# Performance work log

Measured on AMD Instinct MI355X. Metric: run time of the kernel, lower is better.

Reference implementation:

```python
import jax, jax.numpy as jnp
import numpy as np
from jax import lax

B, C_IN, L = 512, 32, 512
E = 8
POOL = 16            # AdaptiveAvgPool1d(16)
D_IN = C_IN * L      # expert input = flattened x
D_OUT = 768          # pooler_output dim (hard-coded in module)
TAU = 1.0            # gumbel temperature
BN_EPS = 1e-5


def setup_inputs() -> dict:
    key = jax.random.key(0)
    ks = jax.random.split(key, 8)
    s = 0.02
    return {
        "x": jax.random.normal(ks[0], (B, C_IN, L), jnp.float32),
        "gumbel_u": jax.random.uniform(ks[1], (B, E), jnp.float32, 1e-6, 1.0 - 1e-6),
        "conv_w": jax.random.normal(ks[2], (64, C_IN, 3), jnp.float32) * s,
        "conv_b": jnp.zeros((64,), jnp.float32),
        "bn_gamma": jnp.ones((64 * POOL,), jnp.float32),
        "bn_beta": jnp.zeros((64 * POOL,), jnp.float32),
        "bn_mean": jnp.zeros((64 * POOL,), jnp.float32),
        "bn_var": jnp.ones((64 * POOL,), jnp.float32),
        "fc1_w": jax.random.normal(ks[3], (128, 64 * POOL), jnp.float32) * s,
        "fc1_b": jnp.zeros((128,), jnp.float32),
        "fc2_w": jax.random.normal(ks[4], (E, 128), jnp.float32) * s,
        "fc2_b": jnp.zeros((E,), jnp.float32),
        "expert_w": jax.random.normal(ks[5], (E, D_IN, D_OUT), jnp.float32) * s,
        "expert_b": jnp.zeros((E, D_OUT), jnp.float32),
    }


def _gelu(v):
    return jax.nn.gelu(v, approximate=False)  # torch nn.GELU default (erf)


def reference(x, gumbel_u, conv_w, conv_b, bn_gamma, bn_beta, bn_mean, bn_var,
              fc1_w, fc1_b, fc2_w, fc2_b, expert_w, expert_b):
    # ---- router ----
    h = lax.conv_general_dilated(x, conv_w, (1,), ((1, 1),),
                                 dimension_numbers=("NCH", "OIH", "NCH"))
    h = _gelu(h + conv_b[None, :, None])                     # [B,64,L]
    h = h.reshape(B, 64, POOL, L // POOL).mean(-1)           # adaptive avg pool -> [B,64,16]
    h = h.reshape(B, 64 * POOL)                              # flatten
    h = (h - bn_mean) * lax.rsqrt(bn_var + BN_EPS) * bn_gamma + bn_beta  # BN (eval)
    h = _gelu(h @ fc1_w.T + fc1_b)                           # dropout inactive in eval
    logits = h @ fc2_w.T + fc2_b                             # [B,E]

    # ---- soft gumbel-softmax gating (hard=False), then top-2 ----
    g = -jnp.log(-jnp.log(gumbel_u))
    routing_weights = jax.nn.softmax((logits + g) / TAU, axis=1)
    topv, topi = lax.top_k(routing_weights, 2)               # [B,2]
    w = topv / (topv.sum(axis=1, keepdims=True) + 1e-8)      # [B,2]

    # ---- dispatch/compute/combine (dense-expert stand-in: flatten + linear) ----
    xf = x.reshape(B, D_IN)
    all_out = jnp.einsum("bd,edh->beh", xf, expert_w) + expert_b[None]  # [B,E,768]
    sel = jnp.take_along_axis(all_out, topi[:, :, None], axis=1)        # [B,2,768]
    pooler_output = (sel * w[:, :, None]).sum(axis=1)                   # [B,768]
    return pooler_output
```

## Files before the change

kernel.cpp:

```cpp
#include <hip/hip_runtime.h>
#include <hip/hip_bf16.h>

#define NB 512
#define CIN 32
#define LEN 512
#define NE 8
#define NPOOL 16
#define DIN 16384
#define DOUT 768
#define HD 1024
#define F1 128

#define MT 256
#define NT 64
#define BK 32
#define NBUF 4

typedef __attribute__((ext_vector_type(4))) float f32x4;
typedef __attribute__((ext_vector_type(8))) short s16x8;
typedef __attribute__((ext_vector_type(4))) unsigned int u32x4;

__device__ __forceinline__ float gelu_erf(float v) {
    return 0.5f * v * (1.0f + erff(v * 0.70710678118654752f));
}

__device__ __forceinline__ unsigned cvt_pk(float lo, float hi) {
    unsigned r;
    asm volatile("v_cvt_pk_bf16_f32 %0, %1, %2" : "=v"(r) : "v"(lo), "v"(hi));
    return r;
}

__device__ __forceinline__ unsigned short f2bf_u(float f) {
    union { float f; unsigned u; } x; x.f = f;
    unsigned r = x.u + 0x7fffu + ((x.u >> 16) & 1u);
    return (unsigned short)(r >> 16);
}

__device__ __forceinline__ void gload_lds16(const void* gptr, void* lptr) {
    __builtin_amdgcn_global_load_lds(
        (const __attribute__((address_space(1))) unsigned int*)gptr,
        (__attribute__((address_space(3))) unsigned int*)lptr,
        16, 0, 0);
}

__global__ __launch_bounds__(256) void krouter_conv(
    const float* __restrict__ x, const float* __restrict__ cw, const float* __restrict__ cb,
    const float* __restrict__ bng, const float* __restrict__ bnb,
    const float* __restrict__ bnm, const float* __restrict__ bnv,
    float* __restrict__ h, int* __restrict__ cnt)
{
    __shared__ float xs[CIN * 264];
    int half = blockIdx.x;
    int b = blockIdx.y;
    int t = threadIdx.x;
    if (b == 0 && half == 0 && t < NE) cnt[t] = 0;

    int Lchunk0 = half * 64 - 1;
    const float* xb_ = x + (size_t)b * DIN;
    for (int idx = t; idx < CIN * 66; idx += 256) {
        int ci = idx / 66;
        int cc = idx - ci * 66;
        int gc = min(max(Lchunk0 + cc, 0), 127);
        f32x4 v = *(const f32x4*)(xb_ + ci * 512 + gc * 4);
        int byte = ci * 1056 + ((cc << 4) ^ (((cc >> 3) & 7) << 4));
        *(f32x4*)((char*)xs + byte) = v;
    }
    __syncthreads();

    int p  = t & 7;
    int pg = half * 8 + p;
    int cq = t >> 3;
    int co0 = cq * 2, co1 = co0 + 1;

    float sa[32], sb[32];
    #pragma unroll
    for (int i = 0; i < 32; ++i) { sa[i] = 0.f; sb[i] = 0.f; }

    for (int ci = 0; ci < CIN; ++ci) {
        float f[40];
        #pragma unroll
        for (int u = 0; u < 10; ++u) {
            int lc = p * 8 + u;
            int byte = ci * 1056 + ((lc << 4) ^ (((lc >> 3) & 7) << 4));
            f32x4 v = *(const f32x4*)((const char*)xs + byte);
            f[4*u+0] = v[0]; f[4*u+1] = v[1]; f[4*u+2] = v[2]; f[4*u+3] = v[3];
        }
        if (pg == 0)  f[3]  = 0.f;
        if (pg == 15) f[36] = 0.f;
        float wa0 = cw[co0*96 + ci*3 + 0], wa1 = cw[co0*96 + ci*3 + 1], wa2 = cw[co0*96 + ci*3 + 2];
        float wb0 = cw[co1*96 + ci*3 + 0], wb1 = cw[co1*96 + ci*3 + 1], wb2 = cw[co1*96 + ci*3 + 2];
        #pragma unroll
        for (int i = 0; i < 32; ++i) {
            sa[i] = fmaf(f[i+3], wa0, fmaf(f[i+4], wa1, fmaf(f[i+5], wa2, sa[i])));
            sb[i] = fmaf(f[i+3], wb0, fmaf(f[i+4], wb1, fmaf(f[i+5], wb2, sb[i])));
        }
    }

    float ba = cb[co0], bbv = cb[co1];
    float ma = 0.f, mb = 0.f;
    #pragma unroll
    for (int i = 0; i < 32; ++i) { ma += gelu_erf(sa[i] + ba); mb += gelu_erf(sb[i] + bbv); }
    ma *= (1.f / 32.f); mb *= (1.f / 32.f);

    int oa = co0 * NPOOL + pg, ob = co1 * NPOOL + pg;
    float ra = (ma - bnm[oa]) * rsqrtf(bnv[oa] + 1e-5f) * bng[oa] + bnb[oa];
    float rb = (mb - bnm[ob]) * rsqrtf(bnv[ob] + 1e-5f) * bng[ob] + bnb[ob];
    h[(size_t)b * HD + oa] = ra;
    h[(size_t)b * HD + ob] = rb;
}

__global__ __launch_bounds__(256) void krouter_fc(
    const float* __restrict__ h, const float* __restrict__ f1w, const float* __restrict__ f1b,
    const float* __restrict__ f2w, const float* __restrict__ f2b,
    const float* __restrict__ gu,
    int* __restrict__ top2e, float* __restrict__ top2w,
    int* __restrict__ cnt, int* __restrict__ rowlist, float* __restrict__ roww)
{
    __shared__ float hs[8 * HD];
    __shared__ float h1s[8 * F1];
    __shared__ float lg[8 * NE];

    int bb = blockIdx.x * 8;
    int t = threadIdx.x;

    const f32x4* hg = (const f32x4*)(h + (size_t)bb * HD);
    f32x4* hs4 = (f32x4*)hs;
    #pragma unroll
    for (int u = 0; u < 8; ++u) hs4[t + 256 * u] = hg[t + 256 * u];
    __syncthreads();

    int j = t & 127;
    int pr = t >> 7;
    float acc[4] = {0.f, 0.f, 0.f, 0.f};
    const f32x4* w4 = (const f32x4*)(f1w + (size_t)j * HD);
    for (int k4 = 0; k4 < 256; ++k4) {
        f32x4 w = w4[k4];
        #pragma unroll
        for (int g = 0; g < 4; ++g) {
            f32x4 hv = hs4[(pr * 4 + g) * 256 + k4];
            acc[g] += w[0]*hv[0] + w[1]*hv[1] + w[2]*hv[2] + w[3]*hv[3];
        }
    }
    float bj = f1b[j];
    #pragma unroll
    for (int g = 0; g < 4; ++g) h1s[(pr * 4 + g) * F1 + j] = gelu_erf(acc[g] + bj);
    __syncthreads();

    if (t < 64) {
        int bi = t >> 3, e = t & 7;
        float s = f2b[e];
        const float* w = f2w + e * F1;
        const float* hh = h1s + bi * F1;
        #pragma unroll 8
        for (int k = 0; k < F1; ++k) s += hh[k] * w[k];
        lg[bi * NE + e] = s;
    }
    __syncthreads();

    if (t < 8) {
        int bi = t; int b = bb + bi;
        float r[NE];
        float mx = -1e30f;
        #pragma unroll
        for (int e = 0; e < NE; ++e) {
            float g = -logf(-logf(gu[b * NE + e]));
            r[e] = lg[bi * NE + e] + g;
            mx = fmaxf(mx, r[e]);
        }
        float sum = 0.f;
        #pragma unroll
        for (int e = 0; e < NE; ++e) { r[e] = expf(r[e] - mx); sum += r[e]; }
        float inv = 1.f / sum;
        #pragma unroll
        for (int e = 0; e < NE; ++e) r[e] *= inv;
        int e0 = 0; float v0 = r[0];
        #pragma unroll
        for (int e = 1; e < NE; ++e) if (r[e] > v0) { v0 = r[e]; e0 = e; }
        int e1 = -1; float v1 = -1.f;
        #pragma unroll
        for (int e = 0; e < NE; ++e) { if (e == e0) continue; if (r[e] > v1) { v1 = r[e]; e1 = e; } }
        float den = v0 + v1 + 1e-8f;
        float w0 = v0 / den, w1 = v1 / den;
        top2e[b * 2 + 0] = e0; top2e[b * 2 + 1] = e1;
        top2w[b * 2 + 0] = w0; top2w[b * 2 + 1] = w1;
        int p0 = atomicAdd(&cnt[e0], 1);
        rowlist[e0 * NB + p0] = b * 2 + 0; roww[e0 * NB + p0] = w0;
        int p1 = atomicAdd(&cnt[e1], 1);
        rowlist[e1 * NB + p1] = b * 2 + 1; roww[e1 * NB + p1] = w1;
    }
}

__global__ __launch_bounds__(512, 4) void kgemm(
    const float* __restrict__ x, const float* __restrict__ ew,
    const int* __restrict__ cnt, const int* __restrict__ rowlist, const float* __restrict__ roww,
    unsigned short* __restrict__ ypart, int nkc, int kch)
{
    int nwg = gridDim.x;
    int cpx = nwg >> 3;
    int wg = (blockIdx.x & 7) * cpx + (blockIdx.x >> 3);
    int nt = wg % 12;
    int kc = (wg / 12) % nkc;
    int e  = wg / (12 * nkc);
    int cn = cnt[e];
    if (cn <= 0) return;

    __shared__ __align__(16) char As[2][MT * 64];
    __shared__ __align__(16) char Bs[NBUF][BK * NT * 4];

    int t = threadIdx.x;
    int wid = t >> 6, lane = t & 63;
    int wm = wid >> 1, wn = wid & 1;
    int g = lane >> 4;
    int NS = kch / BK;
    int k0 = kc * kch;

    const char* gB = (const char*)ew + (size_t)e * DIN * DOUT * 4
                   + (size_t)k0 * (DOUT * 4) + nt * NT * 4;
    int bk_ = wid * 4 + (lane >> 4);
    int bc_ = lane & 15;
    int bkey = ((bk_ >> 3) & 3) << 2;
    const char* gp = gB + (size_t)bk_ * (DOUT * 4) + ((bc_ ^ bkey) << 4);
    int ldsB = wid * 1024;

    int arow = t >> 1, ah = t & 1;
    int akey = (arow ^ (arow >> 2)) & 3;
    int aw0 = arow * 64 + (((2 * ah) ^ akey) << 4);
    int aw1 = arow * 64 + (((2 * ah + 1) ^ akey) << 4);

    for (int row0 = 0; row0 < cn; row0 += MT) {
        int mloc = min(MT, cn - row0);
        bool wact = (wm * 64 < mloc);

        int arc = min(arow, mloc - 1);
        const float* axp = x + (size_t)(rowlist[e * NB + row0 + arc] >> 1) * DIN
                         + k0 + ah * 16;

        f32x4 acc[4][2];
        #pragma unroll
        for (int i = 0; i < 4; ++i)
            #pragma unroll
            for (int jj = 0; jj < 2; ++jj) acc[i][jj] = (f32x4){0.f, 0.f, 0.f, 0.f};

        f32x4 An[4];
        const char* bp = gp;

        auto loadA = [&](int s) {
            const f32x4* p = (const f32x4*)(axp + (size_t)s * BK);
            An[0] = p[0]; An[1] = p[1]; An[2] = p[2]; An[3] = p[3];
        };
        auto stageB = [&](int s) {
            gload_lds16(bp + (size_t)s * ((size_t)BK * DOUT * 4),
                        (char*)Bs[s & (NBUF - 1)] + ldsB);
        };
        auto writeA = [&](int bi) {
            u32x4 q0, q1;
            q0[0] = cvt_pk(An[0][0], An[0][1]); q0[1] = cvt_pk(An[0][2], An[0][3]);
            q0[2] = cvt_pk(An[1][0], An[1][1]); q0[3] = cvt_pk(An[1][2], An[1][3]);
            q1[0] = cvt_pk(An[2][0], An[2][1]); q1[1] = cvt_pk(An[2][2], An[2][3]);
            q1[2] = cvt_pk(An[3][0], An[3][1]); q1[3] = cvt_pk(An[3][2], An[3][3]);
            *(u32x4*)(As[bi] + aw0) = q0;
            *(u32x4*)(As[bi] + aw1) = q1;
        };

        loadA(0);
        stageB(0);
        if (NS > 1) stageB(1);
        writeA(0);

        for (int s = 0; s < NS; ++s) {
            if (s + 1 < NS) loadA(s + 1);
            if (s + 2 < NS) stageB(s + 2);
            __builtin_amdgcn_sched_barrier(0);
            if (s + 2 < NS)      asm volatile("s_waitcnt vmcnt(6) lgkmcnt(0)" ::: "memory");
            else if (s + 1 < NS) asm volatile("s_waitcnt vmcnt(5) lgkmcnt(0)" ::: "memory");
            else                 asm volatile("s_waitcnt vmcnt(0) lgkmcnt(0)" ::: "memory");
            __builtin_amdgcn_sched_barrier(0);
            __builtin_amdgcn_s_barrier();
            __builtin_amdgcn_sched_barrier(0);

            if (wact) {
                const char* Ab = As[s & 1];
                const char* Bb = Bs[s & (NBUF - 1)];
                __builtin_amdgcn_s_setprio(1);
                s16x8 af[4];
                #pragma unroll
                for (int mi = 0; mi < 4; ++mi) {
                    int m = wm * 64 + mi * 16 + (lane & 15);
                    int key = (m ^ (m >> 2)) & 3;
                    af[mi] = *(const s16x8*)(Ab + m * 64 + ((g ^ key) << 4));
                }
                #pragma unroll
                for (int ni = 0; ni < 2; ++ni) {
                    int n = wn * 32 + ni * 16 + (lane & 15);
                    int cb = (((n >> 2) ^ (g << 2)) << 4) + ((n & 3) << 2);
                    float v[8];
                    #pragma unroll
                    for (int j = 0; j < 8; ++j)
                        v[j] = *(const float*)(Bb + (g * 8 + j) * 256 + cb);
                    union { u32x4 u; s16x8 v8; } bf;
                    bf.u[0] = cvt_pk(v[0], v[1]); bf.u[1] = cvt_pk(v[2], v[3]);
                    bf.u[2] = cvt_pk(v[4], v[5]); bf.u[3] = cvt_pk(v[6], v[7]);
                    #pragma unroll
                    for (int mi = 0; mi < 4; ++mi)
                        acc[mi][ni] = __builtin_amdgcn_mfma_f32_16x16x32_bf16(af[mi], bf.v8, acc[mi][ni], 0, 0, 0);
                }
                __builtin_amdgcn_s_setprio(0);
            }
            __builtin_amdgcn_sched_barrier(0);
            if (s + 1 < NS) writeA((s + 1) & 1);
        }

        if (wact) {
            #pragma unroll
            for (int mi = 0; mi < 4; ++mi) {
                #pragma unroll
                for (int rg = 0; rg < 4; ++rg) {
                    int m = wm * 64 + mi * 16 + g * 4 + rg;
                    if (m < mloc) {
                        int ent = rowlist[e * NB + row0 + m];
                        float wgt = roww[e * NB + row0 + m];
                        int ob = ent >> 1, slot = ent & 1;
                        unsigned short* dst = ypart + ((size_t)(slot * nkc + kc) * NB + ob) * DOUT
                                            + nt * NT + wn * 32 + (lane & 15);
                        #pragma unroll
                        for (int ni = 0; ni < 2; ++ni)
                            dst[ni * 16] = f2bf_u(acc[mi][ni][rg] * wgt);
                    }
                }
            }
        }
        asm volatile("s_waitcnt vmcnt(0) lgkmcnt(0)" ::: "memory");
        __builtin_amdgcn_s_barrier();
    }
}

__global__ __launch_bounds__(256) void kcombine(
    const unsigned short* __restrict__ ypart,
    const int* __restrict__ top2e, const float* __restrict__ top2w,
    const float* __restrict__ eb, float* __restrict__ out, int nplanes)
{
    int b = blockIdx.y;
    int n = blockIdx.x * 256 + threadIdx.x;
    float s = 0.f;
    for (int p = 0; p < nplanes; ++p) {
        unsigned v = ypart[((size_t)p * NB + b) * DOUT + n];
        union { unsigned u; float f; } c; c.u = v << 16;
        s += c.f;
    }
    int e0 = top2e[b * 2], e1 = top2e[b * 2 + 1];
    float w0 = top2w[b * 2], w1 = top2w[b * 2 + 1];
    s += w0 * eb[e0 * DOUT + n] + w1 * eb[e1 * DOUT + n];
    out[(size_t)b * DOUT + n] = s;
}

extern "C" void kernel_launch(void* const* d_in, const int* in_sizes, int n_in,
                              void* d_out, int out_size, void* d_ws, size_t ws_size,
                              hipStream_t stream)
{
    const float* x   = (const float*)d_in[0];
    const float* gu  = (const float*)d_in[1];
    const float* cw  = (const float*)d_in[2];
    const float* cb  = (const float*)d_in[3];
    const float* bng = (const float*)d_in[4];
    const float* bnb = (const float*)d_in[5];
    const float* bnm = (const float*)d_in[6];
    const float* bnv = (const float*)d_in[7];
    const float* f1w = (const float*)d_in[8];
    const float* f1b = (const float*)d_in[9];
    const float* f2w = (const float*)d_in[10];
    const float* f2b = (const float*)d_in[11];
    const float* ew  = (const float*)d_in[12];
    const float* eb  = (const float*)d_in[13];

    int nkc = (ws_size >= (size_t)40 * 1024 * 1024) ? 16 : 8;
    int kch = DIN / nkc;

    char* ws = (char*)d_ws;
    size_t off = 0;
    float* h       = (float*)(ws + off); off += (size_t)NB * HD * 4;
    int*   top2e   = (int*)(ws + off);   off += (size_t)NB * 2 * 4;
    float* top2w   = (float*)(ws + off); off += (size_t)NB * 2 * 4;
    int*   cnt     = (int*)(ws + off);   off += 256;
    int*   rowlist = (int*)(ws + off);   off += (size_t)NE * NB * 4;
    float* roww    = (float*)(ws + off); off += (size_t)NE * NB * 4;
    unsigned short* ypart = (unsigned short*)(ws + off);
    off += (size_t)2 * nkc * NB * DOUT * 2;

    krouter_conv<<<dim3(2, NB), 256, 0, stream>>>(x, cw, cb, bng, bnb, bnm, bnv, h, cnt);
    krouter_fc<<<NB / 8, 256, 0, stream>>>(h, f1w, f1b, f2w, f2b, gu,
                                           top2e, top2w, cnt, rowlist, roww);
    kgemm<<<NE * nkc * 12, 512, 0, stream>>>(x, ew, cnt, rowlist, roww, ypart, nkc, kch);
    kcombine<<<dim3(3, NB), 256, 0, stream>>>(ypart, top2e, top2w, eb, (float*)d_out, 2 * nkc);
}
```

Measured before the change: 259.8 us.

## Pre-convert x to bf16 and widen the GEMM N tile with async A loads

Adds a kernel that converts x to bf16 in workspace before the expert GEMM. The GEMM can then stage A tiles straight into LDS with global_load_lds into a 4-deep buffer, instead of loading fp32 into registers and converting per step. The N tile doubles from 64 to 128, halving the workgroup count and the repeated A reads, and occupancy is lowered to 2 to fit the larger accumulators. The cost is an extra full pass over x (32 MB read, 16 MB write) plus a larger workspace, which raises the threshold for using 16 K-chunks.

```diff
diff --git a/kernel.cpp b/kernel.cpp
--- a/kernel.cpp
+++ b/kernel.cpp
@@ -12,7 +12,7 @@
 #define F1 128
 
 #define MT 256
-#define NT 64
+#define NT 128
 #define BK 32
 #define NBUF 4
 
@@ -41,6 +41,18 @@
         (const __attribute__((address_space(1))) unsigned int*)gptr,
         (__attribute__((address_space(3))) unsigned int*)lptr,
         16, 0, 0);
+}
+
+__global__ __launch_bounds__(256) void kcvt(const float* __restrict__ x,
+                                            unsigned short* __restrict__ xb)
+{
+    int i = blockIdx.x * 256 + threadIdx.x;
+    const f32x4* src = (const f32x4*)(x + (size_t)i * 8);
+    f32x4 v0 = src[0], v1 = src[1];
+    u32x4 pk;
+    pk[0] = cvt_pk(v0[0], v0[1]); pk[1] = cvt_pk(v0[2], v0[3]);
+    pk[2] = cvt_pk(v1[0], v1[1]); pk[3] = cvt_pk(v1[2], v1[3]);
+    *(u32x4*)(xb + (size_t)i * 8) = pk;
 }
 
 __global__ __launch_bounds__(256) void krouter_conv(
@@ -190,21 +202,21 @@
     }
 }
 
-__global__ __launch_bounds__(512, 4) void kgemm(
-    const float* __restrict__ x, const float* __restrict__ ew,
+__global__ __launch_bounds__(512, 2) void kgemm(
+    const unsigned short* __restrict__ xb, const float* __restrict__ ew,
     const int* __restrict__ cnt, const int* __restrict__ rowlist, const float* __restrict__ roww,
     unsigned short* __restrict__ ypart, int nkc, int kch)
 {
     int nwg = gridDim.x;
     int cpx = nwg >> 3;
     int wg = (blockIdx.x & 7) * cpx + (blockIdx.x >> 3);
-    int nt = wg % 12;
-    int kc = (wg / 12) % nkc;
-    int e  = wg / (12 * nkc);
+    int nt = wg % 6;
+    int kc = (wg / 6) % nkc;
+    int e  = wg / (6 * nkc);
     int cn = cnt[e];
     if (cn <= 0) return;
 
-    __shared__ __align__(16) char As[2][MT * 64];
+    __shared__ __align__(16) char As[NBUF][MT * 64];
     __shared__ __align__(16) char Bs[NBUF][BK * NT * 4];
 
     int t = threadIdx.x;
@@ -216,87 +228,84 @@
 
     const char* gB = (const char*)ew + (size_t)e * DIN * DOUT * 4
                    + (size_t)k0 * (DOUT * 4) + nt * NT * 4;
-    int bk_ = wid * 4 + (lane >> 4);
-    int bc_ = lane & 15;
-    int bkey = ((bk_ >> 3) & 3) << 2;
-    const char* gp = gB + (size_t)bk_ * (DOUT * 4) + ((bc_ ^ bkey) << 4);
-    int ldsB = wid * 1024;
-
-    int arow = t >> 1, ah = t & 1;
-    int akey = (arow ^ (arow >> 2)) & 3;
-    int aw0 = arow * 64 + (((2 * ah) ^ akey) << 4);
-    int aw1 = arow * 64 + (((2 * ah + 1) ^ akey) << 4);
+    int keyb = wid >> 1;
+    int brow0 = wid * 4 + (lane >> 5);
+    const char* gpB0 = gB + (size_t)brow0 * (DOUT * 4) + ((size_t)((lane & 31) ^ keyb) << 4);
+    const char* gpB1 = gpB0 + 2 * (DOUT * 4);
+    int ldsB0 = wid * 2048, ldsB1 = wid * 2048 + 1024;
+
+    int keya = ((lane >> 2) ^ (lane >> 4)) & 3;
+    int aq = (lane & 3) ^ keya;
+    int ldsA0 = wid * 2048, ldsA1 = wid * 2048 + 1024;
+
+    int af_off[4];
+    #pragma unroll
+    for (int mi = 0; mi < 4; ++mi) {
+        int m = wm * 64 + mi * 16 + (lane & 15);
+        int key = ((m & 3) ^ ((m >> 2) & 3));
+        af_off[mi] = m * 64 + ((g ^ key) << 4);
+    }
+    int cb[4];
+    #pragma unroll
+    for (int ni = 0; ni < 4; ++ni) {
+        int n = wn * 64 + ni * 16 + (lane & 15);
+        cb[ni] = (((n >> 2) ^ g) << 4) + ((n & 3) << 2);
+    }
 
     for (int row0 = 0; row0 < cn; row0 += MT) {
         int mloc = min(MT, cn - row0);
         bool wact = (wm * 64 < mloc);
 
-        int arc = min(arow, mloc - 1);
-        const float* axp = x + (size_t)(rowlist[e * NB + row0 + arc] >> 1) * DIN
-                         + k0 + ah * 16;
-
-        f32x4 acc[4][2];
+        int r0 = wid * 32 + (lane >> 2);
+        int r1 = r0 + 16;
+        size_t ab0 = (size_t)(rowlist[e * NB + row0 + min(r0, mloc - 1)] >> 1) * (DIN * 2);
+        size_t ab1 = (size_t)(rowlist[e * NB + row0 + min(r1, mloc - 1)] >> 1) * (DIN * 2);
+        const char* gpA0 = (const char*)xb + ab0 + (size_t)k0 * 2 + (aq << 4);
+        const char* gpA1 = (const char*)xb + ab1 + (size_t)k0 * 2 + (aq << 4);
+
+        f32x4 acc[4][4];
         #pragma unroll
         for (int i = 0; i < 4; ++i)
             #pragma unroll
-            for (int jj = 0; jj < 2; ++jj) acc[i][jj] = (f32x4){0.f, 0.f, 0.f, 0.f};
-
-        f32x4 An[4];
-        const char* bp = gp;
-
-        auto loadA = [&](int s) {
-            const f32x4* p = (const f32x4*)(axp + (size_t)s * BK);
-            An[0] = p[0]; An[1] = p[1]; An[2] = p[2]; An[3] = p[3];
+            for (int jj = 0; jj < 4; ++jj) acc[i][jj] = (f32x4){0.f, 0.f, 0.f, 0.f};
+
+        auto stage = [&](int s) {
+            int bi = s & (NBUF - 1);
+            size_t bo = (size_t)s * (BK * DOUT * 4);
+            gload_lds16(gpB0 + bo, (char*)Bs[bi] + ldsB0);
+            gload_lds16(gpB1 + bo, (char*)Bs[bi] + ldsB1);
+            size_t ao = (size_t)s * (BK * 2);
+            gload_lds16(gpA0 + ao, (char*)As[bi] + ldsA0);
+            gload_lds16(gpA1 + ao, (char*)As[bi] + ldsA1);
         };
-        auto stageB = [&](int s) {
-            gload_lds16(bp + (size_t)s * ((size_t)BK * DOUT * 4),
-                        (char*)Bs[s & (NBUF - 1)] + ldsB);
-        };
-        auto writeA = [&](int bi) {
-            u32x4 q0, q1;
-            q0[0] = cvt_pk(An[0][0], An[0][1]); q0[1] = cvt_pk(An[0][2], An[0][3]);
-            q0[2] = cvt_pk(An[1][0], An[1][1]); q0[3] = cvt_pk(An[1][2], An[1][3]);
-            q1[0] = cvt_pk(An[2][0], An[2][1]); q1[1] = cvt_pk(An[2][2], An[2][3]);
-            q1[2] = cvt_pk(An[3][0], An[3][1]); q1[3] = cvt_pk(An[3][2], An[3][3]);
-            *(u32x4*)(As[bi] + aw0) = q0;
-            *(u32x4*)(As[bi] + aw1) = q1;
-        };
-
-        loadA(0);
-        stageB(0);
-        if (NS > 1) stageB(1);
-        writeA(0);
+
+        stage(0);
+        if (1 < NS) stage(1);
 
         for (int s = 0; s < NS; ++s) {
-            if (s + 1 < NS) loadA(s + 1);
-            if (s + 2 < NS) stageB(s + 2);
+            if (s + 2 < NS) stage(s + 2);
             __builtin_amdgcn_sched_barrier(0);
-            if (s + 2 < NS)      asm volatile("s_waitcnt vmcnt(6) lgkmcnt(0)" ::: "memory");
-            else if (s + 1 < NS) asm volatile("s_waitcnt vmcnt(5) lgkmcnt(0)" ::: "memory");
-            else                 asm volatile("s_waitcnt vmcnt(0) lgkmcnt(0)" ::: "memory");
+            if (s + 2 < NS)      asm volatile("s_waitcnt vmcnt(8)" ::: "memory");
+            else if (s + 1 < NS) asm volatile("s_waitcnt vmcnt(4)" ::: "memory");
+            else                 asm volatile("s_waitcnt vmcnt(0)" ::: "memory");
             __builtin_amdgcn_sched_barrier(0);
             __builtin_amdgcn_s_barrier();
             __builtin_amdgcn_sched_barrier(0);
 
             if (wact) {
-                const char* Ab = As[s & 1];
+                const char* Ab = As[s & (NBUF - 1)];
                 const char* Bb = Bs[s & (NBUF - 1)];
                 __builtin_amdgcn_s_setprio(1);
                 s16x8 af[4];
                 #pragma unroll
-                for (int mi = 0; mi < 4; ++mi) {
-                    int m = wm * 64 + mi * 16 + (lane & 15);
-                    int key = (m ^ (m >> 2)) & 3;
-                    af[mi] = *(const s16x8*)(Ab + m * 64 + ((g ^ key) << 4));
-                }
+                for (int mi = 0; mi < 4; ++mi)
+                    af[mi] = *(const s16x8*)(Ab + af_off[mi]);
                 #pragma unroll
-                for (int ni = 0; ni < 2; ++ni) {
-                    int n = wn * 32 + ni * 16 + (lane & 15);
-                    int cb = (((n >> 2) ^ (g << 2)) << 4) + ((n & 3) << 2);
+                for (int ni = 0; ni < 4; ++ni) {
                     float v[8];
                     #pragma unroll
                     for (int j = 0; j < 8; ++j)
-                        v[j] = *(const float*)(Bb + (g * 8 + j) * 256 + cb);
+                        v[j] = *(const float*)(Bb + g * 4096 + j * 512 + cb[ni]);
                     union { u32x4 u; s16x8 v8; } bf;
                     bf.u[0] = cvt_pk(v[0], v[1]); bf.u[1] = cvt_pk(v[2], v[3]);
                     bf.u[2] = cvt_pk(v[4], v[5]); bf.u[3] = cvt_pk(v[6], v[7]);
@@ -306,8 +315,6 @@
                 }
                 __builtin_amdgcn_s_setprio(0);
             }
-            __builtin_amdgcn_sched_barrier(0);
-            if (s + 1 < NS) writeA((s + 1) & 1);
         }
 
         if (wact) {
@@ -321,9 +328,9 @@
                         float wgt = roww[e * NB + row0 + m];
                         int ob = ent >> 1, slot = ent & 1;
                         unsigned short* dst = ypart + ((size_t)(slot * nkc + kc) * NB + ob) * DOUT
-                                            + nt * NT + wn * 32 + (lane & 15);
+                                            + nt * NT + wn * 64 + (lane & 15);
                         #pragma unroll
-                        for (int ni = 0; ni < 2; ++ni)
+                        for (int ni = 0; ni < 4; ++ni)
                             dst[ni * 16] = f2bf_u(acc[mi][ni][rg] * wgt);
                     }
                 }
@@ -372,7 +379,7 @@
     const float* ew  = (const float*)d_in[12];
     const float* eb  = (const float*)d_in[13];
 
-    int nkc = (ws_size >= (size_t)40 * 1024 * 1024) ? 16 : 8;
+    int nkc = (ws_size >= (size_t)48 * 1024 * 1024) ? 16 : 8;
     int kch = DIN / nkc;
 
     char* ws = (char*)d_ws;
@@ -383,12 +390,15 @@
     int*   cnt     = (int*)(ws + off);   off += 256;
     int*   rowlist = (int*)(ws + off);   off += (size_t)NE * NB * 4;
     float* roww    = (float*)(ws + off); off += (size_t)NE * NB * 4;
+    unsigned short* xbuf = (unsigned short*)(ws + off);
+    off += (size_t)NB * DIN * 2;
     unsigned short* ypart = (unsigned short*)(ws + off);
     off += (size_t)2 * nkc * NB * DOUT * 2;
 
+    kcvt<<<NB * DIN / 8 / 256, 256, 0, stream>>>(x, xbuf);
     krouter_conv<<<dim3(2, NB), 256, 0, stream>>>(x, cw, cb, bng, bnb, bnm, bnv, h, cnt);
     krouter_fc<<<NB / 8, 256, 0, stream>>>(h, f1w, f1b, f2w, f2b, gu,
                                            top2e, top2w, cnt, rowlist, roww);
-    kgemm<<<NE * nkc * 12, 512, 0, stream>>>(x, ew, cnt, rowlist, roww, ypart, nkc, kch);
+    kgemm<<<NE * nkc * 6, 512, 0, stream>>>(xbuf, ew, cnt, rowlist, roww, ypart, nkc, kch);
     kcombine<<<dim3(3, NB), 256, 0, stream>>>(ypart, top2e, top2w, eb, (float*)d_out, 2 * nkc);
 }
```

Result: faster. 253.4 us (-2.5%).
